# Kernel optimization log

Measured on AMD Instinct MI355X. Metric: run time of the kernel, lower is better.

The kernel has to match this reference:

```python
import jax, jax.numpy as jnp
import numpy as np

HEADS = 8

def setup_inputs() -> dict:
    key = jax.random.key(0)
    ks = jax.random.split(key, 6)
    b, c, w, h = 4, 512, 48, 48
    qc, vc = 512, 512
    s = 1.0 / np.sqrt(c)  # orthogonal-init-like scale for 1x1 conv weights
    return {
        "x": jax.random.normal(ks[0], (b, c, w, h), dtype=jnp.float32),
        "Wq": jax.random.normal(ks[1], (qc, c), dtype=jnp.float32) * s,
        "Wk": jax.random.normal(ks[2], (qc, c), dtype=jnp.float32) * s,
        "Wv": jax.random.normal(ks[3], (vc, c), dtype=jnp.float32) * s,
        "Wsc": jax.random.normal(ks[4], (vc, c), dtype=jnp.float32) * s,
        "gamma": jax.random.normal(ks[5], (1, vc, 1, 1), dtype=jnp.float32),
    }


def reference(x, Wq, Wk, Wv, Wsc, gamma):
    b, c, w, h = x.shape
    n = w * h
    dq = Wq.shape[0] // HEADS
    dv = Wv.shape[0] // HEADS
    # 1x1 convs are channel matmuls
    q = jnp.einsum('bchw,oc->bohw', x, Wq).reshape(b, HEADS, dq, n)
    k = jnp.einsum('bchw,oc->bohw', x, Wk).reshape(b, HEADS, dq, n)
    v = jnp.einsum('bchw,oc->bohw', x, Wv).reshape(b, HEADS, dv, n)
    # attention scores over spatial tokens (no scaling in original)
    attn = jax.nn.softmax(jnp.einsum('bhdn,bhdm->bhnm', q, k), axis=-1)
    out = jnp.einsum('bhnm,bhdm->bnhd', attn, v)  # (b, n, heads, dv)
    out = out.reshape(b, w, h, HEADS * dv).transpose(0, 3, 1, 2)  # head-major channels
    sc = jnp.einsum('bchw,oc->bohw', x, Wsc)
    return gamma * out + sc
```

## Files before the change

kernel.cpp:

```cpp
#include <hip/hip_runtime.h>

#define HEADS 8
static constexpr int BSZ = 4;
static constexpr int CCH = 512;
static constexpr int NSP = 2304;
static constexpr int DH  = 64;

typedef _Float16 f16x8 __attribute__((ext_vector_type(8)));
typedef float f32x4 __attribute__((ext_vector_type(4)));
typedef float f32x16 __attribute__((ext_vector_type(16)));
typedef int i32x4 __attribute__((ext_vector_type(4)));
typedef unsigned short u16;
typedef unsigned int u32;

__device__ __forceinline__ u16 f2h(float f) {
  _Float16 h = (_Float16)f;
  return __builtin_bit_cast(u16, h);
}

__device__ __forceinline__ float fexp2(float x) {
  return __builtin_amdgcn_exp2f(x);
}

__device__ __forceinline__ void gl_lds16(const void* g, void* l) {
  __builtin_amdgcn_global_load_lds(
      (const __attribute__((address_space(1))) u32*)g,
      (__attribute__((address_space(3))) u32*)l, 16, 0, 0);
}

__global__ void k_cvt_w(const float* __restrict__ w0, const float* __restrict__ w1,
                        const float* __restrict__ w2, const float* __restrict__ w3,
                        u16* __restrict__ dst) {
  int wsel = blockIdx.y;
  const float* src = wsel == 0 ? w0 : wsel == 1 ? w1 : wsel == 2 ? w2 : w3;
  int i = (blockIdx.x * 256 + threadIdx.x) * 4;
  float4 v = *(const float4*)(src + i);
  ushort4 o;
  o.x = f2h(v.x); o.y = f2h(v.y); o.z = f2h(v.z); o.w = f2h(v.w);
  *(ushort4*)(dst + (size_t)wsel * CCH * CCH + i) = o;
}

__global__ void k_cvt_x(const float* __restrict__ x, u16* __restrict__ xT) {
  __shared__ u16 t[64][66];
  int b = blockIdx.z, c0 = blockIdx.y * 64, n0 = blockIdx.x * 64;
  int col = threadIdx.x & 63, rb = threadIdx.x >> 6;
#pragma unroll
  for (int rr = 0; rr < 16; rr++) {
    int r = rr * 4 + rb;
    t[r][col] = f2h(x[((size_t)b * CCH + c0 + r) * NSP + n0 + col]);
  }
  __syncthreads();
#pragma unroll
  for (int rr = 0; rr < 16; rr++) {
    int r = rr * 4 + rb;
    xT[((size_t)b * NSP + n0 + r) * CCH + c0 + col] = t[col][r];
  }
}

__global__ __launch_bounds__(256) void k_proj(const u16* __restrict__ Wall,
    const u16* __restrict__ xT, u16* __restrict__ Qo, u16* __restrict__ Ko,
    u16* __restrict__ Vo, float* __restrict__ SCo) {
  __shared__ u16 smem[17408];
  u16* At = smem;
  u16* Bt = smem + 8192;
  int z = blockIdx.z, b = z >> 2, wsel = z & 3;
  int o0 = blockIdx.y * 128, n0 = blockIdx.x * 128;
  int tid = threadIdx.x, lane = tid & 63, wv = tid >> 6;
  int wr = wv >> 1, wc = wv & 1;
  const u16* Asrc = Wall + (size_t)wsel * CCH * CCH + (size_t)o0 * CCH;
  const u16* Bsrc = xT + ((size_t)b * NSP + n0) * CCH;
  f32x4 acc[4][4] = {};
  for (int kc = 0; kc < CCH; kc += 64) {
    __syncthreads();
#pragma unroll
    for (int i = 0; i < 4; i++) {
      int ch = (wv * 4 + i) * 64 + lane;
      int row = ch >> 3, cc = ch & 7;
      gl_lds16(Asrc + (size_t)row * CCH + kc + ((cc ^ (row & 7)) << 3), At + (wv * 4 + i) * 512);
      gl_lds16(Bsrc + (size_t)row * CCH + kc + ((cc ^ (row & 7)) << 3), Bt + (wv * 4 + i) * 512);
    }
    __syncthreads();
#pragma unroll
    for (int ks = 0; ks < 2; ks++) {
      f16x8 af[4], bfr[4];
#pragma unroll
      for (int f = 0; f < 4; f++) {
        int orow = wr * 64 + f * 16 + (lane & 15);
        int nrow = wc * 64 + f * 16 + (lane & 15);
        int k8 = (lane >> 4) + ks * 4;
        af[f]  = *(const f16x8*)(At + orow * 64 + ((k8 ^ (orow & 7)) << 3));
        bfr[f] = *(const f16x8*)(Bt + nrow * 64 + ((k8 ^ (nrow & 7)) << 3));
      }
#pragma unroll
      for (int i = 0; i < 4; i++)
#pragma unroll
        for (int j = 0; j < 4; j++)
          acc[i][j] = __builtin_amdgcn_mfma_f32_16x16x32_f16(af[i], bfr[j], acc[i][j], 0, 0, 0);
    }
  }
  if (wsel >= 2) {
#pragma unroll
    for (int i = 0; i < 4; i++)
#pragma unroll
      for (int j = 0; j < 4; j++)
#pragma unroll
        for (int r = 0; r < 4; r++) {
          int o = o0 + wr * 64 + i * 16 + ((lane >> 4) << 2) + r;
          int n = n0 + wc * 64 + j * 16 + (lane & 15);
          size_t idx = ((size_t)b * CCH + o) * NSP + n;
          if (wsel == 3) SCo[idx] = acc[i][j][r];
          else           Vo[idx]  = f2h(acc[i][j][r]);
        }
  } else {
    __syncthreads();
    u16* stash = smem;
    float qs = (wsel == 0) ? 1.4426950408889634f : 1.0f;
#pragma unroll
    for (int i = 0; i < 4; i++)
#pragma unroll
      for (int j = 0; j < 4; j++)
#pragma unroll
        for (int r = 0; r < 4; r++) {
          int ol = wr * 64 + i * 16 + ((lane >> 4) << 2) + r;
          int nl = wc * 64 + j * 16 + (lane & 15);
          stash[nl * 136 + ol] = f2h(acc[i][j][r] * qs);
        }
    __syncthreads();
    u16* dst = wsel ? Ko : Qo;
    int hl = tid >> 7, nn = tid & 127;
    int h = (o0 >> 6) + hl;
    size_t base = ((size_t)(b * HEADS + h) * NSP + n0 + nn) * DH;
#pragma unroll
    for (int c2 = 0; c2 < 8; c2++)
      *(int4*)(dst + base + c2 * 8) = *(const int4*)(stash + nn * 136 + hl * 64 + c2 * 8);
  }
}

__global__ __launch_bounds__(512) void k_attn(const u16* __restrict__ Qw,
    const u16* __restrict__ Kw, const u16* __restrict__ Vw,
    const float* __restrict__ gamma, float* __restrict__ out) {
  __shared__ u16 smem[17408];
  int bh = blockIdx.x, qt = blockIdx.y;
  int b = bh >> 3, h = bh & 7;
  int tid = threadIdx.x, lane = tid & 63, wv = tid >> 6;
  int l31 = lane & 31, hi = lane >> 5;
  int qh = wv & 3, tp = wv >> 2;
  int gid = tid & 255;
  int q0w = qt * 128 + qh * 32;
  const u16* Ksrc = Kw + (size_t)bh * NSP * DH;
  const u16* Vsrc = Vw + ((size_t)b * CCH + h * DH) * NSP;
  u16* PB = smem + tp * 8192;

  int mk = gid >> 3, pk = gid & 7;
  const u16* kc = Ksrc + (tp * 32 + mk) * DH + ((pk ^ (mk & 7)) << 3);
  int dv = gid >> 2, pv = gid & 3;
  const u16* vc = Vsrc + (size_t)dv * NSP + tp * 32 + ((pv ^ ((dv >> 1) & 3)) << 3);

#define STAGE(c)                                   \
  do {                                             \
    gl_lds16(kc, PB + (c) * 4096 + gid * 8);       \
    gl_lds16(vc, PB + (c) * 4096 + 2048 + gid * 8);\
    kc += 64 * DH;                                 \
    vc += 64;                                      \
  } while (0)

#define WAITV(n) asm volatile("s_waitcnt vmcnt(" #n ")" ::: "memory")
#define BARRIER()                          \
  do {                                     \
    __builtin_amdgcn_s_barrier();          \
    __builtin_amdgcn_sched_barrier(0);     \
  } while (0)

  int kswz = l31 & 7, vswz = (l31 >> 1) & 3;
  int kro = l31 * 64;
  int ko[4], vo[2];
#pragma unroll
  for (int kd = 0; kd < 4; kd++) ko[kd] = ((2 * kd + hi) ^ kswz) << 3;
#pragma unroll
  for (int s = 0; s < 2; s++) vo[s] = ((2 * s + hi) ^ vswz) << 3;
  int vr0 = l31 * 32, vr1 = (32 + l31) * 32;

  f16x8 qf[4];
  const u16* Qbase = Qw + ((size_t)bh * NSP + q0w + l31) * DH + hi * 8;
#pragma unroll
  for (int kd = 0; kd < 4; kd++)
    qf[kd] = *(const f16x8*)(Qbase + kd * 16);

  float mrun = -1e30f, lrun = 0.f;
  f32x16 acc0 = {}, acc1 = {};

#define COMPUTE(c)                                                           \
  do {                                                                       \
    const u16* Kc = PB + (c) * 4096;                                         \
    const u16* Vc = Kc + 2048;                                               \
    f32x16 s0 = {};                                                          \
    __builtin_amdgcn_s_setprio(1);                                           \
    _Pragma("unroll")                                                        \
    for (int kd = 0; kd < 4; kd++) {                                         \
      f16x8 k0 = *(const f16x8*)(Kc + kro + ko[kd]);                         \
      s0 = __builtin_amdgcn_mfma_f32_32x32x16_f16(k0, qf[kd], s0, 0, 0, 0);  \
    }                                                                        \
    __builtin_amdgcn_s_setprio(0);                                           \
    float m0a = fmaxf(fmaxf(s0[0], s0[1]), s0[2]);                           \
    float m0b = fmaxf(fmaxf(s0[3], s0[4]), s0[5]);                           \
    float m0c = fmaxf(fmaxf(s0[6], s0[7]), s0[8]);                           \
    float m0d = fmaxf(fmaxf(s0[9], s0[10]), s0[11]);                         \
    float m0e = fmaxf(fmaxf(s0[12], s0[13]), s0[14]);                        \
    float tm = fmaxf(fmaxf(fmaxf(m0a, m0b), fmaxf(m0c, m0d)),                \
                     fmaxf(m0e, s0[15]));                                    \
    tm = fmaxf(tm, __shfl_xor(tm, 32));                                      \
    if (__any(tm > mrun + 11.5f)) {                                          \
      float mnew = fmaxf(mrun, tm);                                          \
      float scl = fexp2(mrun - mnew);                                        \
      mrun = mnew;                                                           \
      lrun *= scl;                                                           \
      _Pragma("unroll")                                                      \
      for (int r = 0; r < 16; r++) {                                         \
        float sq = __shfl(scl, (r & 3) + 8 * (r >> 2) + 4 * hi);             \
        acc0[r] *= sq;                                                       \
        acc1[r] *= sq;                                                       \
      }                                                                      \
    }                                                                        \
    float ts = 0.f;                                                          \
    u32 P2[4][2];                                                            \
    _Pragma("unroll")                                                        \
    for (int s2 = 0; s2 < 4; s2++)                                           \
      _Pragma("unroll")                                                      \
      for (int c2 = 0; c2 < 2; c2++) {                                       \
        float a = fexp2(s0[4 * s2 + 2 * c2] - mrun);                         \
        float bb = fexp2(s0[4 * s2 + 2 * c2 + 1] - mrun);                    \
        ts += a + bb;                                                        \
        P2[s2][c2] = __builtin_bit_cast(u32, __builtin_amdgcn_cvt_pkrtz(a, bb)); \
      }                                                                      \
    ts += __shfl_xor(ts, 32);                                                \
    lrun += ts;                                                              \
    _Pragma("unroll")                                                        \
    for (int s = 0; s < 2; s++) {                                            \
      int x0 = (int)P2[2 * s][0], y0 = (int)P2[2 * s + 1][0];                \
      int x1 = (int)P2[2 * s][1], y1 = (int)P2[2 * s + 1][1];                \
      asm("v_permlane32_swap_b32 %0, %1" : "+v"(x0), "+v"(y0));              \
      asm("v_permlane32_swap_b32 %0, %1" : "+v"(x1), "+v"(y1));              \
      f16x8 pa = __builtin_bit_cast(f16x8, (i32x4){x0, x1, y0, y1});         \
      __builtin_amdgcn_s_setprio(1);                                         \
      {                                                                      \
        f16x8 vb = *(const f16x8*)(Vc + vr0 + vo[s]);                        \
        acc0 = __builtin_amdgcn_mfma_f32_32x32x16_f16(pa, vb, acc0, 0, 0, 0);\
      }                                                                      \
      {                                                                      \
        f16x8 vb = *(const f16x8*)(Vc + vr1 + vo[s]);                        \
        acc1 = __builtin_amdgcn_mfma_f32_32x32x16_f16(pa, vb, acc1, 0, 0, 0);\
      }                                                                      \
      __builtin_amdgcn_s_setprio(0);                                         \
    }                                                                        \
  } while (0)

  STAGE(0);
  for (int i2 = 0; i2 < 18; i2++) {
    STAGE(1);
    WAITV(2);
    BARRIER();
    COMPUTE(0);
    BARRIER();
    if (i2 < 17) {
      STAGE(0);
      WAITV(2);
    } else {
      WAITV(0);
    }
    BARRIER();
    COMPUTE(1);
    BARRIER();
  }

  float* sf = (float*)smem;
  if (tp) {
#pragma unroll
    for (int r = 0; r < 16; r++) {
      sf[qh * 2048 + r * 64 + lane] = acc0[r];
      sf[qh * 2048 + (16 + r) * 64 + lane] = acc1[r];
    }
    if (lane < 32) {
      sf[8192 + qh * 64 + l31] = mrun;
      sf[8192 + qh * 64 + 32 + l31] = lrun;
    }
  }
  __syncthreads();
  if (!tp) {
    float mb = sf[8192 + qh * 64 + l31];
    float lb = sf[8192 + qh * 64 + 32 + l31];
    float M = fmaxf(mrun, mb);
    float fa = fexp2(mrun - M), fb = fexp2(mb - M);
    float linv = 1.0f / (lrun * fa + lb * fb);
    fa *= linv; fb *= linv;
    float faq[16], fbq[16];
#pragma unroll
    for (int r = 0; r < 16; r++) {
      int qloc = (r & 3) + 8 * (r >> 2) + 4 * hi;
      faq[r] = __shfl(fa, qloc);
      fbq[r] = __shfl(fb, qloc);
    }
    size_t outbase = ((size_t)b * CCH + h * DH) * NSP;
#pragma unroll
    for (int dblk = 0; dblk < 2; dblk++) {
      int d = dblk * 32 + l31;
      float g = gamma[h * DH + d];
      float* orow = out + outbase + (size_t)d * NSP + q0w;
#pragma unroll
      for (int s2 = 0; s2 < 4; s2++) {
        int n = 8 * s2 + 4 * hi;
        f32x4 o;
#pragma unroll
        for (int t = 0; t < 4; t++) {
          int r = 4 * s2 + t;
          float oa = dblk ? acc1[r] : acc0[r];
          float ob = sf[qh * 2048 + (dblk * 16 + r) * 64 + lane];
          o[t] = (oa * faq[r] + ob * fbq[r]) * g;
        }
        f32x4 sc = *(const f32x4*)(orow + n);
        *(f32x4*)(orow + n) = o + sc;
      }
    }
  }
#undef STAGE
#undef COMPUTE
#undef WAITV
#undef BARRIER
}

extern "C" void kernel_launch(void* const* d_in, const int* in_sizes, int n_in,
                              void* d_out, int out_size, void* d_ws, size_t ws_size,
                              hipStream_t stream) {
  const float* x     = (const float*)d_in[0];
  const float* Wq    = (const float*)d_in[1];
  const float* Wk    = (const float*)d_in[2];
  const float* Wv    = (const float*)d_in[3];
  const float* Wsc   = (const float*)d_in[4];
  const float* gamma = (const float*)d_in[5];
  float* out = (float*)d_out;

  u16* xT   = (u16*)d_ws;
  u16* Wall = xT + (size_t)BSZ * NSP * CCH;
  u16* Qw   = Wall + (size_t)4 * CCH * CCH;
  u16* Kw   = Qw + (size_t)BSZ * CCH * NSP;
  u16* Vw   = Kw + (size_t)BSZ * CCH * NSP;

  hipLaunchKernelGGL(k_cvt_w, dim3(CCH * CCH / 1024, 4), dim3(256), 0, stream,
                     Wq, Wk, Wv, Wsc, Wall);
  hipLaunchKernelGGL(k_cvt_x, dim3(NSP / 64, CCH / 64, BSZ), dim3(256), 0, stream, x, xT);
  hipLaunchKernelGGL(k_proj, dim3(NSP / 128, CCH / 128, BSZ * 4), dim3(256), 0, stream,
                     Wall, xT, Qw, Kw, Vw, out);
  hipLaunchKernelGGL(k_attn, dim3(BSZ * HEADS, NSP / 128), dim3(512), 0, stream,
                     Qw, Kw, Vw, gamma, out);
}
```

Baseline: 144.9 us.

## Software-pipeline QK^T ahead of softmax/PV with triple-buffered LDS stages

Splits the attention inner step into a QK^T MFMA phase and a softmax+PV phase. The next tile's QK^T is now issued before the current tile's softmax and PV, so MFMA work can overlap the exp and shuffle work. LDS grows from two to three K/V stage buffers per wave group, with rotating buffer offsets. The cost is more LDS per block, which may cut occupancy, and an extra live score accumulator that raises register pressure.

```diff
diff --git a/kernel.cpp b/kernel.cpp
--- a/kernel.cpp
+++ b/kernel.cpp
@@ -139,7 +139,7 @@
 __global__ __launch_bounds__(512) void k_attn(const u16* __restrict__ Qw,
     const u16* __restrict__ Kw, const u16* __restrict__ Vw,
     const float* __restrict__ gamma, float* __restrict__ out) {
-  __shared__ u16 smem[17408];
+  __shared__ u16 smem[24576];
   int bh = blockIdx.x, qt = blockIdx.y;
   int b = bh >> 3, h = bh & 7;
   int tid = threadIdx.x, lane = tid & 63, wv = tid >> 6;
@@ -149,7 +149,7 @@
   int q0w = qt * 128 + qh * 32;
   const u16* Ksrc = Kw + (size_t)bh * NSP * DH;
   const u16* Vsrc = Vw + ((size_t)b * CCH + h * DH) * NSP;
-  u16* PB = smem + tp * 8192;
+  u16* PB = smem + tp * 12288;
 
   int mk = gid >> 3, pk = gid & 7;
   const u16* kc = Ksrc + (tp * 32 + mk) * DH + ((pk ^ (mk & 7)) << 3);
@@ -158,8 +158,8 @@
 
 #define STAGE(c)                                   \
   do {                                             \
-    gl_lds16(kc, PB + (c) * 4096 + gid * 8);       \
-    gl_lds16(vc, PB + (c) * 4096 + 2048 + gid * 8);\
+    gl_lds16(kc, PB + (c) + gid * 8);              \
+    gl_lds16(vc, PB + (c) + 2048 + gid * 8);       \
     kc += 64 * DH;                                 \
     vc += 64;                                      \
   } while (0)
@@ -188,26 +188,31 @@
 
   float mrun = -1e30f, lrun = 0.f;
   f32x16 acc0 = {}, acc1 = {};
-
-#define COMPUTE(c)                                                           \
+  const f32x16 kZero = {};
+
+#define QK(S, c)                                                             \
   do {                                                                       \
-    const u16* Kc = PB + (c) * 4096;                                         \
-    const u16* Vc = Kc + 2048;                                               \
-    f32x16 s0 = {};                                                          \
+    const u16* Kc = PB + (c);                                                \
+    S = kZero;                                                               \
     __builtin_amdgcn_s_setprio(1);                                           \
     _Pragma("unroll")                                                        \
     for (int kd = 0; kd < 4; kd++) {                                         \
       f16x8 k0 = *(const f16x8*)(Kc + kro + ko[kd]);                         \
-      s0 = __builtin_amdgcn_mfma_f32_32x32x16_f16(k0, qf[kd], s0, 0, 0, 0);  \
+      S = __builtin_amdgcn_mfma_f32_32x32x16_f16(k0, qf[kd], S, 0, 0, 0);    \
     }                                                                        \
     __builtin_amdgcn_s_setprio(0);                                           \
-    float m0a = fmaxf(fmaxf(s0[0], s0[1]), s0[2]);                           \
-    float m0b = fmaxf(fmaxf(s0[3], s0[4]), s0[5]);                           \
-    float m0c = fmaxf(fmaxf(s0[6], s0[7]), s0[8]);                           \
-    float m0d = fmaxf(fmaxf(s0[9], s0[10]), s0[11]);                         \
-    float m0e = fmaxf(fmaxf(s0[12], s0[13]), s0[14]);                        \
+  } while (0)
+
+#define SMPV(S, c)                                                           \
+  do {                                                                       \
+    const u16* Vc = PB + (c) + 2048;                                         \
+    float m0a = fmaxf(fmaxf(S[0], S[1]), S[2]);                              \
+    float m0b = fmaxf(fmaxf(S[3], S[4]), S[5]);                              \
+    float m0c = fmaxf(fmaxf(S[6], S[7]), S[8]);                              \
+    float m0d = fmaxf(fmaxf(S[9], S[10]), S[11]);                            \
+    float m0e = fmaxf(fmaxf(S[12], S[13]), S[14]);                           \
     float tm = fmaxf(fmaxf(fmaxf(m0a, m0b), fmaxf(m0c, m0d)),                \
-                     fmaxf(m0e, s0[15]));                                    \
+                     fmaxf(m0e, S[15]));                                     \
     tm = fmaxf(tm, __shfl_xor(tm, 32));                                      \
     if (__any(tm > mrun + 11.5f)) {                                          \
       float mnew = fmaxf(mrun, tm);                                          \
@@ -227,8 +232,8 @@
     for (int s2 = 0; s2 < 4; s2++)                                           \
       _Pragma("unroll")                                                      \
       for (int c2 = 0; c2 < 2; c2++) {                                       \
-        float a = fexp2(s0[4 * s2 + 2 * c2] - mrun);                         \
-        float bb = fexp2(s0[4 * s2 + 2 * c2 + 1] - mrun);                    \
+        float a = fexp2(S[4 * s2 + 2 * c2] - mrun);                          \
+        float bb = fexp2(S[4 * s2 + 2 * c2 + 1] - mrun);                     \
         ts += a + bb;                                                        \
         P2[s2][c2] = __builtin_bit_cast(u32, __builtin_amdgcn_cvt_pkrtz(a, bb)); \
       }                                                                      \
@@ -241,36 +246,51 @@
       asm("v_permlane32_swap_b32 %0, %1" : "+v"(x0), "+v"(y0));              \
       asm("v_permlane32_swap_b32 %0, %1" : "+v"(x1), "+v"(y1));              \
       f16x8 pa = __builtin_bit_cast(f16x8, (i32x4){x0, x1, y0, y1});         \
+      int pvx = vo[s];                                                       \
       __builtin_amdgcn_s_setprio(1);                                         \
       {                                                                      \
-        f16x8 vb = *(const f16x8*)(Vc + vr0 + vo[s]);                        \
+        f16x8 vb = *(const f16x8*)(Vc + vr0 + pvx);                          \
         acc0 = __builtin_amdgcn_mfma_f32_32x32x16_f16(pa, vb, acc0, 0, 0, 0);\
       }                                                                      \
       {                                                                      \
-        f16x8 vb = *(const f16x8*)(Vc + vr1 + vo[s]);                        \
+        f16x8 vb = *(const f16x8*)(Vc + vr1 + pvx);                          \
         acc1 = __builtin_amdgcn_mfma_f32_32x32x16_f16(pa, vb, acc1, 0, 0, 0);\
       }                                                                      \
       __builtin_amdgcn_s_setprio(0);                                         \
     }                                                                        \
   } while (0)
 
-  STAGE(0);
-  for (int i2 = 0; i2 < 18; i2++) {
-    STAGE(1);
+  f32x16 sA = {}, sB = {};
+  int cA = 0, cB = 4096, cC = 8192;
+
+  STAGE(cA);
+  STAGE(cB);
+  WAITV(2);
+  BARRIER();
+  QK(sA, cA);
+
+  for (int t2 = 0; t2 < 17; t2++) {
+    STAGE(cC);
     WAITV(2);
     BARRIER();
-    COMPUTE(0);
+    QK(sB, cB);
+    SMPV(sA, cA);
     BARRIER();
-    if (i2 < 17) {
-      STAGE(0);
-      WAITV(2);
-    } else {
-      WAITV(0);
-    }
+    { int tmp = cA; cA = cB; cB = cC; cC = tmp; }
+    STAGE(cC);
+    WAITV(2);
     BARRIER();
-    COMPUTE(1);
+    QK(sA, cB);
+    SMPV(sB, cA);
     BARRIER();
-  }
+    { int tmp = cA; cA = cB; cB = cC; cC = tmp; }
+  }
+  WAITV(0);
+  BARRIER();
+  QK(sB, cB);
+  SMPV(sA, cA);
+  SMPV(sB, cB);
+  BARRIER();
 
   float* sf = (float*)smem;
   if (tp) {
@@ -322,7 +342,8 @@
     }
   }
 #undef STAGE
-#undef COMPUTE
+#undef QK
+#undef SMPV
 #undef WAITV
 #undef BARRIER
 }
```

Result: slower. 163.3 us (+12.7%).
